# Kernel optimization log

Measured on AMD Instinct MI355X. Metric: run time of the kernel, lower is better.

The kernel has to match this reference:

```python
import jax, jax.numpy as jnp
import numpy as np

E, H, F = 1024, 16, 4096
WH, WW = 32, 32
B = 4
L = WH * WW           # 1024 cross-attn kv tokens
N = L + 1             # 1025 decoder tokens (CLS + window)
D = E // H
SCALE = D ** -0.5
NEG = -1e9            # stands in for -inf in the causal mask


def _rel_coords(Wh, Ww):
    coords = np.stack(np.meshgrid(np.arange(Wh), np.arange(Ww), indexing='ij')).reshape(2, -1)
    rc = (coords[:, :, None] - coords[:, None, :]).transpose(1, 2, 0).astype(np.int64)
    rc[:, :, 0] += Wh - 1
    rc[:, :, 1] += Ww - 1
    rc[:, :, 0] *= 2 * Ww - 1
    return rc.sum(-1)  # (L, L)


def rel_index_self(Wh, Ww):
    nrd = (2 * Wh - 1) * (2 * Ww - 1) + 3
    l = Wh * Ww
    idx = np.zeros((l + 1, l + 1), dtype=np.int32)
    idx[1:, 1:] = _rel_coords(Wh, Ww)
    idx[0, :] = nrd - 3
    idx[:, 0] = nrd - 2
    idx[0, 0] = nrd - 1
    return idx


def rel_index_cross(Wh, Ww):
    nrd = (2 * Wh - 1) * (2 * Ww - 1) + 1
    l = Wh * Ww
    idx = np.zeros((l + 1, l), dtype=np.int32)
    idx[1:, :] = _rel_coords(Wh, Ww)
    idx[0, :] = nrd - 1
    return idx


IDX_SELF = jnp.asarray(rel_index_self(WH, WW))    # (N, N) int32
IDX_CROSS = jnp.asarray(rel_index_cross(WH, WW))  # (N, L) int32
CAUSAL = jnp.triu(jnp.full((N, N), NEG, jnp.float32), 1)


def _ln(x, g, b, eps=1e-5):
    m = x.mean(-1, keepdims=True)
    v = ((x - m) ** 2).mean(-1, keepdims=True)
    return (x - m) * jax.lax.rsqrt(v + eps) * g + b


def setup_inputs():
    key = jax.random.key(0)
    ks = jax.random.split(key, 24)
    g = lambda i, shape, s=0.02: jax.random.normal(ks[i], shape, jnp.float32) * s
    return dict(
        x=g(0, (B, N, E), 1.0),
        y=g(1, (B, L, E), 1.0),
        norm1_g=jnp.ones((E,), jnp.float32), norm1_b=jnp.zeros((E,), jnp.float32),
        norm2_g=jnp.ones((E,), jnp.float32), norm2_b=jnp.zeros((E,), jnp.float32),
        norm3_g=jnp.ones((E,), jnp.float32), norm3_b=jnp.zeros((E,), jnp.float32),
        sa_qkv_w=g(2, (3 * E, E)),
        sa_q_bias=g(3, (E,)),
        sa_v_bias=g(4, (E,)),
        sa_rpb=g(5, ((2 * WH - 1) * (2 * WW - 1) + 3, H)),
        sa_proj_w=g(6, (E, E)), sa_proj_b=g(7, (E,)),
        ca_q_w=g(8, (E, E)),
        ca_kv_w=g(9, (2 * E, E)),
        ca_q_bias=g(10, (E,)),
        ca_v_bias=g(11, (E,)),
        ca_rpb=g(12, ((2 * WH - 1) * (2 * WW - 1) + 1, H)),
        ca_proj_w=g(13, (E, E)), ca_proj_b=g(14, (E,)),
        fc1_w=g(15, (F, E)), fc1_b=g(16, (F,)),
        fc2_w=g(17, (E, F)), fc2_b=g(18, (E,)),
        gamma1=jnp.full((E,), 0.1, jnp.float32),
        gamma2=jnp.full((E,), 0.1, jnp.float32),
        gamma3=jnp.full((E,), 0.1, jnp.float32),
    )


def reference(x, y, norm1_g, norm1_b, norm2_g, norm2_b, norm3_g, norm3_b,
              sa_qkv_w, sa_q_bias, sa_v_bias, sa_rpb, sa_proj_w, sa_proj_b,
              ca_q_w, ca_kv_w, ca_q_bias, ca_v_bias, ca_rpb, ca_proj_w, ca_proj_b,
              fc1_w, fc1_b, fc2_w, fc2_b, gamma1, gamma2, gamma3):
    # cross_attn.extract_kv(y): k gets zero bias, v gets v_bias
    kv_bias = jnp.concatenate([jnp.zeros((E,), x.dtype), ca_v_bias])
    kv = (y @ ca_kv_w.T + kv_bias).reshape(B, L, 2, H, D)
    ck = kv[:, :, 0].transpose(0, 2, 1, 3)  # (B,H,L,D)
    cv = kv[:, :, 1].transpose(0, 2, 1, 3)

    # --- causal self-attention with gathered relative-position bias ---
    h = _ln(x, norm1_g, norm1_b)
    qkv_bias = jnp.concatenate([sa_q_bias, jnp.zeros((E,), x.dtype), sa_v_bias])
    qkv = (h @ sa_qkv_w.T + qkv_bias).reshape(B, N, 3, H, D)
    q = qkv[:, :, 0].transpose(0, 2, 1, 3) * SCALE  # (B,H,N,D)
    k = qkv[:, :, 1].transpose(0, 2, 1, 3)
    v = qkv[:, :, 2].transpose(0, 2, 1, 3)
    bias = sa_rpb[IDX_SELF].transpose(2, 0, 1) + CAUSAL  # (H,N,N)
    attn = jnp.einsum('bhqd,bhkd->bhqk', q, k) + bias[None]
    attn = jax.nn.softmax(attn, axis=-1)
    sa = jnp.einsum('bhqk,bhkd->bhqd', attn, v).transpose(0, 2, 1, 3).reshape(B, N, E)
    sa = sa @ sa_proj_w.T + sa_proj_b
    x = x + gamma1 * sa

    # --- cross-attention with gathered relative-position bias ---
    h = _ln(x, norm2_g, norm2_b)
    q = (h @ ca_q_w.T + ca_q_bias).reshape(B, N, H, D).transpose(0, 2, 1, 3) * SCALE
    cbias = ca_rpb[IDX_CROSS].transpose(2, 0, 1)  # (H,N,L)
    attn = jnp.einsum('bhqd,bhkd->bhqk', q, ck) + cbias[None]
    attn = jax.nn.softmax(attn, axis=-1)
    ca = jnp.einsum('bhqk,bhkd->bhqd', attn, cv).transpose(0, 2, 1, 3).reshape(B, N, E)
    ca = ca @ ca_proj_w.T + ca_proj_b
    x = x + gamma2 * ca

    # --- FFN (Linear -> GELU -> Linear, no inner identity) ---
    h = _ln(x, norm3_g, norm3_b)
    h = jax.nn.gelu(h @ fc1_w.T + fc1_b, approximate=False)
    h = h @ fc2_w.T + fc2_b
    x = x + gamma3 * h
    return x
```

## Files before the change

kernel.cpp:

```cpp
#include <hip/hip_runtime.h>
#include <hip/hip_bf16.h>
#include <math.h>

typedef __bf16 bf16;
typedef __bf16 bf16x8 __attribute__((ext_vector_type(8)));
typedef float f32x4 __attribute__((ext_vector_type(4)));

#define MP    4224
#define MACT  4100
#define NQTOK 1025
#define NKTOK 1024
#define EDIM  1024
#define FDIM  4096
#define NHEAD 16
#define HD    64
#define QSCALE 0.125f
#define VTS   1056

__device__ __forceinline__ void glds16(const bf16* g, bf16* l) {
  __builtin_amdgcn_global_load_lds(
      (const __attribute__((address_space(1))) void*)g,
      (__attribute__((address_space(3))) void*)l, 16, 0, 0);
}

__device__ __forceinline__ bf16x8 ld8(const void* p, size_t i, bool f32) {
  if (f32) {
    const float* q = (const float*)p + i;
    bf16x8 r;
#pragma unroll
    for (int j = 0; j < 8; ++j) r[j] = (bf16)q[j];
    return r;
  }
  return *(const bf16x8*)((const bf16*)p + i);
}

struct WPtrs { const float* s[8]; };
__global__ __launch_bounds__(256) void conv_kernel(WPtrs wp, bf16* dst) {
  const size_t sz[8] = {3145728UL, 1048576UL, 1048576UL, 2097152UL,
                        1048576UL, 4194304UL, 4194304UL, 4194304UL};
  size_t id = ((size_t)blockIdx.x * 256 + threadIdx.x) * 8;
  size_t off = 0;
#pragma unroll
  for (int i = 0; i < 8; ++i) {
    if (id < off + sz[i]) {
      const float* s = wp.s[i] + (id - off);
      bf16x8 r;
#pragma unroll
      for (int j = 0; j < 8; ++j) r[j] = (bf16)s[j];
      *(bf16x8*)(dst + id) = r;
      return;
    }
    off += sz[i];
  }
}

__global__ void zero_pads_kernel(bf16* hln) {
  int i = blockIdx.x * 256 + threadIdx.x;
  const int n = (MP - MACT) * EDIM;
  if (i < n) hln[(size_t)MACT * EDIM + i] = (bf16)0.0f;
}

template<bool FIRST>
__global__ __launch_bounds__(256) void ln_kernel(const float* __restrict__ src,
    float* __restrict__ xf, bf16* __restrict__ out,
    const float* __restrict__ g, const float* __restrict__ bta) {
  const int row = blockIdx.x;
  const int tid = threadIdx.x;
  float v[4];
#pragma unroll
  for (int i = 0; i < 4; ++i) {
    v[i] = src[(size_t)row * EDIM + tid + i * 256];
    if (FIRST) xf[(size_t)row * EDIM + tid + i * 256] = v[i];
  }
  float s = 0.f, sq = 0.f;
#pragma unroll
  for (int i = 0; i < 4; ++i) { s += v[i]; sq += v[i] * v[i]; }
#pragma unroll
  for (int m = 32; m >= 1; m >>= 1) {
    s += __shfl_xor(s, m);
    sq += __shfl_xor(sq, m);
  }
  __shared__ float ss[4], ssq[4];
  const int wave = tid >> 6;
  if ((tid & 63) == 0) { ss[wave] = s; ssq[wave] = sq; }
  __syncthreads();
  s = ss[0] + ss[1] + ss[2] + ss[3];
  sq = ssq[0] + ssq[1] + ssq[2] + ssq[3];
  const float mean = s * (1.f / EDIM);
  const float var = sq * (1.f / EDIM) - mean * mean;
  const float rstd = rsqrtf(var + 1e-5f);
#pragma unroll
  for (int i = 0; i < 4; ++i) {
    int e = tid + i * 256;
    out[(size_t)row * EDIM + e] = (bf16)((v[i] - mean) * rstd * g[e] + bta[e]);
  }
}

__global__ __launch_bounds__(256) void fc2_reduce_kernel(
    const float* __restrict__ p0, const float* __restrict__ xf,
    const float* __restrict__ bias, const float* __restrict__ gamma,
    float* __restrict__ outf) {
  size_t i = ((size_t)blockIdx.x * 256 + threadIdx.x) * 4;
  if (i >= (size_t)MACT * EDIM) return;
  f32x4 a = *(const f32x4*)(p0 + i);
  f32x4 b = *(const f32x4*)(outf + i);
  f32x4 x = *(const f32x4*)(xf + i);
  const int gn = (int)(i & (EDIM - 1));
  f32x4 r;
#pragma unroll
  for (int j = 0; j < 4; ++j)
    r[j] = x[j] + gamma[gn + j] * (a[j] + b[j] + bias[gn + j]);
  *(f32x4*)(outf + i) = r;
}

enum { EPI_QKV = 0, EPI_KV = 1, EPI_Q = 2, EPI_RES = 3, EPI_GELU = 4,
       EPI_FINAL = 5, EPI_PART = 6 };

template<int EPI, bool ASY>
__global__ __launch_bounds__(256) void gemm_bt(
    const void* __restrict__ A, const void* __restrict__ Bw,
    int K, int Kc,
    const float* __restrict__ bias0, const float* __restrict__ bias1,
    const float* __restrict__ gamma, float* __restrict__ xf,
    bf16* __restrict__ out0, bf16* __restrict__ out1, bf16* __restrict__ out2,
    float* __restrict__ outf)
{
  constexpr int LDP = ASY ? 32 : 40;
  __shared__ bf16 As[2][128][LDP];
  __shared__ bf16 Bs[2][128][LDP];
  const int tid = threadIdx.x;
  const int lane = tid & 63, wave = tid >> 6;
  const int quad = lane >> 4, l16 = lane & 15;
  const int wr = wave >> 1, wc = wave & 1;
  const int m0 = blockIdx.y * 128, n0 = blockIdx.x * 128;
  const int kbase = blockIdx.z * Kc;
  const bool first = (blockIdx.z == 0);
  const int r0 = tid >> 2, c0 = (tid & 3) * 8;

  const bf16* gA = nullptr; const bf16* gB = nullptr;
  if (ASY) {
    gA = (const bf16*)A + (size_t)(m0 + wave * 16 + (lane >> 2)) * K + kbase + (lane & 3) * 8;
    gB = (const bf16*)Bw + (size_t)(n0 + wave * 16 + (lane >> 2)) * K + kbase + (lane & 3) * 8;
  }

  auto stage = [&](int bi, int kk) {
    if (ASY) {
      const bf16* pA = gA + kk;
      const bf16* pB = gB + kk;
      bf16* la = &As[bi][wave * 16][0];
      bf16* lb = &Bs[bi][wave * 16][0];
      glds16(pA, la);
      glds16(pA + (size_t)64 * K, la + 64 * LDP);
      glds16(pB, lb);
      glds16(pB + (size_t)64 * K, lb + 64 * LDP);
    } else {
      const bool f32a = (EPI == EPI_KV);
      const size_t kkk = (size_t)(kbase + kk);
      *(bf16x8*)(&As[bi][r0][c0])      = ld8(A,  (size_t)(m0 + r0) * K + kkk + c0, f32a);
      *(bf16x8*)(&As[bi][r0 + 64][c0]) = ld8(A,  (size_t)(m0 + r0 + 64) * K + kkk + c0, f32a);
      *(bf16x8*)(&Bs[bi][r0][c0])      = ld8(Bw, (size_t)(n0 + r0) * K + kkk + c0, true);
      *(bf16x8*)(&Bs[bi][r0 + 64][c0]) = ld8(Bw, (size_t)(n0 + r0 + 64) * K + kkk + c0, true);
    }
  };

  f32x4 acc[4][4];
#pragma unroll
  for (int i = 0; i < 4; ++i)
#pragma unroll
    for (int j = 0; j < 4; ++j)
#pragma unroll
      for (int r = 0; r < 4; ++r) acc[i][j][r] = 0.f;

  stage(0, 0);
  __syncthreads();
  int buf = 0;
  for (int k0 = 0; k0 < Kc; k0 += 32) {
    if (k0 + 32 < Kc) stage(buf ^ 1, k0 + 32);
    bf16x8 af[4], bfv[4];
#pragma unroll
    for (int i = 0; i < 4; ++i) {
      af[i]  = *(const bf16x8*)(&As[buf][wr * 64 + i * 16 + l16][quad * 8]);
      bfv[i] = *(const bf16x8*)(&Bs[buf][wc * 64 + i * 16 + l16][quad * 8]);
    }
#pragma unroll
    for (int mb = 0; mb < 4; ++mb)
#pragma unroll
      for (int nb = 0; nb < 4; ++nb)
        acc[mb][nb] = __builtin_amdgcn_mfma_f32_16x16x32_bf16(af[mb], bfv[nb], acc[mb][nb], 0, 0, 0);
    __syncthreads();
    buf ^= 1;
  }

#pragma unroll
  for (int mb = 0; mb < 4; ++mb) {
#pragma unroll
    for (int r = 0; r < 4; ++r) {
      const int gm = m0 + wr * 64 + mb * 16 + quad * 4 + r;
#pragma unroll
      for (int nb = 0; nb < 4; ++nb) {
        const int gn = n0 + wc * 64 + nb * 16 + l16;
        float v = acc[mb][nb][r];
        if (EPI == EPI_QKV) {
          if (gm < MACT) {
            unsigned b = (unsigned)gm / 1025u;
            unsigned t = (unsigned)gm - b * 1025u;
            int sec = gn >> 10, e = gn & 1023;
            int h = e >> 6, d = e & 63;
            if (sec == 0)
              out0[((size_t)(b * NHEAD + h) * NQTOK + t) * HD + d] =
                  (bf16)((v + bias0[e]) * QSCALE);
            else if (sec == 1)
              out1[((size_t)(b * NHEAD + h) * NQTOK + t) * HD + d] = (bf16)v;
            else
              out2[((size_t)(b * NHEAD + h) * HD + d) * VTS + t] =
                  (bf16)(v + bias1[e]);
          }
        } else if (EPI == EPI_KV) {
          unsigned b = (unsigned)gm >> 10;
          unsigned t = (unsigned)gm & 1023u;
          int sec = gn >> 10, e = gn & 1023;
          int h = e >> 6, d = e & 63;
          if (sec == 0)
            out0[((size_t)(b * NHEAD + h) * NKTOK + t) * HD + d] = (bf16)v;
          else
            out1[((size_t)(b * NHEAD + h) * HD + d) * NKTOK + t] =
                (bf16)(v + bias1[e]);
        } else if (EPI == EPI_Q) {
          if (gm < MACT) {
            unsigned b = (unsigned)gm / 1025u;
            unsigned t = (unsigned)gm - b * 1025u;
            int h = gn >> 6, d = gn & 63;
            outf[((size_t)(b * NHEAD + h) * NQTOK + t) * HD + d] =
                (v + bias0[gn]) * QSCALE;
          }
        } else if (EPI == EPI_RES) {
          if (gm < MACT) {
            size_t o = (size_t)gm * EDIM + gn;
            xf[o] += gamma[gn] * (v + bias0[gn]);
          }
        } else if (EPI == EPI_GELU) {
          float z = v + bias0[gn];
          float ge = 0.5f * z * (1.0f + erff(z * 0.70710678118f));
          out0[(size_t)gm * FDIM + gn] = (bf16)ge;
        } else if (EPI == EPI_PART) {
          if (gm < MACT) {
            float* dst = first ? xf : outf;
            dst[(size_t)gm * EDIM + gn] = v;
          }
        } else {
          if (gm < MACT) {
            size_t o = (size_t)gm * EDIM + gn;
            float add = gamma[gn] * (v + (first ? bias0[gn] : 0.f));
            if (first) add += xf[o];
            atomicAdd(&outf[o], add);
          }
        }
      }
    }
  }
}

template<bool CROSS>
__global__ __launch_bounds__(256) void attn_kernel(
    const void* __restrict__ Q, const bf16* __restrict__ Kg,
    const bf16* __restrict__ Vg, const float* __restrict__ rpb,
    bf16* __restrict__ out)
{
  const int NK  = CROSS ? NKTOK : NQTOK;
  const int NRD = CROSS ? 3970 : 3972;
  const int VS  = CROSS ? NKTOK : VTS;
  const int qt  = CROSS ? blockIdx.x : (16 - blockIdx.x);
  const int h = blockIdx.y, b = blockIdx.z;
  const int tid = threadIdx.x;
  const int lane = tid & 63, wave = tid >> 6;
  const int quad = lane >> 4, l16 = lane & 15;

  __shared__ bf16 rpb_s[4096];
  __shared__ bf16 Ks[64][72];
  __shared__ bf16 Vt[64][72];

  for (int i = tid; i < 4096; i += 256)
    rpb_s[i] = (bf16)((i < NRD) ? rpb[(size_t)i * NHEAD + h] : 0.f);

  const int q0 = qt * 64;
  const int qrow = q0 + wave * 16 + l16;
  const size_t qhb = (size_t)(b * NHEAD + h) * NQTOK;
  bf16x8 qf0, qf1;
  if (qrow < NQTOK) {
    if (CROSS) {
      const float* Qf = (const float*)Q + (qhb + qrow) * HD;
#pragma unroll
      for (int j = 0; j < 8; ++j) {
        qf0[j] = (bf16)Qf[quad * 8 + j];
        qf1[j] = (bf16)Qf[32 + quad * 8 + j];
      }
    } else {
      const bf16* Qb = (const bf16*)Q;
      qf0 = *(const bf16x8*)(Qb + (qhb + qrow) * HD + quad * 8);
      qf1 = *(const bf16x8*)(Qb + (qhb + qrow) * HD + 32 + quad * 8);
    }
  } else {
#pragma unroll
    for (int j = 0; j < 8; ++j) { qf0[j] = (bf16)0.f; qf1[j] = (bf16)0.f; }
  }

  const int qg = qrow;
  const int qp = qg - 1;
  const int qcode = (qg > 0) ? ((qp >> 5) * 63 + (qp & 31) + 1984) : 0;

  int ib[4][4];
#pragma unroll
  for (int kb = 0; kb < 4; ++kb)
#pragma unroll
    for (int r = 0; r < 4; ++r) {
      const int o = kb * 16 + quad * 4 + r;
      const int om = CROSS ? o : (o - 1);
      const int ocode = (om >> 5) * 63 + (om & 31);
      ib[kb][r] = qcode - ocode;
    }
  const bool q0cls = (q0 == 0);

  float m_run = -1e30f, l_run = 0.f;
  f32x4 oacc[4];
#pragma unroll
  for (int d = 0; d < 4; ++d)
#pragma unroll
    for (int r = 0; r < 4; ++r) oacc[d][r] = 0.f;

  const size_t kvbK = (size_t)(b * NHEAD + h) * NK;
  const size_t vbase = (size_t)(b * NHEAD + h) * HD;
  const int nch = CROSS ? (NKTOK / 64) : (qt + 1);

  const int rr = tid >> 3;
  const int co = (tid & 7) * 8;

  const int srcA = (quad & 1) * 32 + l16;
  const int srcB = srcA + 16;

  bf16x8 krg[2], vrg[2];
  auto stage_load = [&](int c) {
    const int kc = c * 64;
#pragma unroll
    for (int vv = 0; vv < 2; ++vv) {
      const int row = rr + vv * 32;
      if (!CROSS && kc + row >= NK) {
#pragma unroll
        for (int j = 0; j < 8; ++j) krg[vv][j] = (bf16)0.f;
      } else {
        krg[vv] = *(const bf16x8*)(Kg + (kvbK + kc + row) * HD + co);
      }
      if (!CROSS && kc + co >= NK) {
#pragma unroll
        for (int j = 0; j < 8; ++j) vrg[vv][j] = (bf16)0.f;
      } else {
        vrg[vv] = *(const bf16x8*)(Vg + (vbase + row) * VS + kc + co);
      }
    }
  };

  stage_load(0);
  int c126 = 0;
  for (int c = 0; c < nch; ++c) {
    const int kc = c * 64;
    if (c) __syncthreads();
#pragma unroll
    for (int vv = 0; vv < 2; ++vv) {
      const int row = rr + vv * 32;
      *(bf16x8*)(&Ks[row][co]) = krg[vv];
      *(bf16x8*)(&Vt[row][co]) = vrg[vv];
    }
    __syncthreads();
    if (c + 1 < nch) stage_load(c + 1);

    f32x4 aacc[4];
    __builtin_amdgcn_s_setprio(1);
#pragma unroll
    for (int kb = 0; kb < 4; ++kb) {
      bf16x8 kf0 = *(const bf16x8*)(&Ks[kb * 16 + l16][quad * 8]);
      bf16x8 kf1 = *(const bf16x8*)(&Ks[kb * 16 + l16][32 + quad * 8]);
      f32x4 a;
#pragma unroll
      for (int r = 0; r < 4; ++r) a[r] = 0.f;
      a = __builtin_amdgcn_mfma_f32_16x16x32_bf16(kf0, qf0, a, 0, 0, 0);
      a = __builtin_amdgcn_mfma_f32_16x16x32_bf16(kf1, qf1, a, 0, 0, 0);
      aacc[kb] = a;
    }
    __builtin_amdgcn_s_setprio(0);

    float sv[4][4];
    const bool lastc = (!CROSS) && (c == nch - 1);
    const bool firstc = (c == 0);
    if (!lastc) {
#pragma unroll
      for (int kb = 0; kb < 4; ++kb)
#pragma unroll
        for (int r = 0; r < 4; ++r) {
          int idx = ib[kb][r] - c126;
          if (q0cls) { if (qg == 0) idx = 3969; }
          if (!CROSS && firstc && kb == 0 && r == 0) {
            if (quad == 0) idx = (qg == 0) ? 3971 : 3970;
          }
          idx &= 4095;
          sv[kb][r] = aacc[kb][r] + (float)rpb_s[idx];
        }
    } else {
#pragma unroll
      for (int kb = 0; kb < 4; ++kb)
#pragma unroll
        for (int r = 0; r < 4; ++r) {
          int idx = ib[kb][r] - c126;
          if (q0cls) { if (qg == 0) idx = 3969; }
          if (firstc && kb == 0 && r == 0) {
            if (quad == 0) idx = (qg == 0) ? 3971 : 3970;
          }
          idx &= 4095;
          const int kg = kc + kb * 16 + quad * 4 + r;
          const bool valid = (kg < NK) && (kg <= qg);
          sv[kb][r] = valid ? (aacc[kb][r] + (float)rpb_s[idx]) : -1e30f;
        }
    }
    c126 += 126;

    float mx = sv[0][0];
#pragma unroll
    for (int kb = 0; kb < 4; ++kb)
#pragma unroll
      for (int r = 0; r < 4; ++r) mx = fmaxf(mx, sv[kb][r]);
    mx = fmaxf(mx, __shfl_xor(mx, 16));
    mx = fmaxf(mx, __shfl_xor(mx, 32));

    if (!__all(mx - m_run <= 8.f)) {
      const float mnew = fmaxf(m_run, mx);
      const float alpha = __expf(m_run - mnew);
      m_run = mnew;
      l_run *= alpha;
      float alr[4];
#pragma unroll
      for (int r = 0; r < 4; ++r) alr[r] = __shfl(alpha, quad * 4 + r);
#pragma unroll
      for (int d = 0; d < 4; ++d)
#pragma unroll
        for (int r = 0; r < 4; ++r) oacc[d][r] *= alr[r];
    }

    float rs = 0.f;
    unsigned pk[4][2];
#pragma unroll
    for (int kb = 0; kb < 4; ++kb) {
      float p0 = __expf(sv[kb][0] - m_run);
      float p1 = __expf(sv[kb][1] - m_run);
      float p2 = __expf(sv[kb][2] - m_run);
      float p3 = __expf(sv[kb][3] - m_run);
      rs += (p0 + p1) + (p2 + p3);
      union { __bf16 h[2]; unsigned u; } w0, w1;
      w0.h[0] = (bf16)p0; w0.h[1] = (bf16)p1;
      w1.h[0] = (bf16)p2; w1.h[1] = (bf16)p3;
      pk[kb][0] = w0.u; pk[kb][1] = w1.u;
    }
    rs += __shfl_xor(rs, 16);
    rs += __shfl_xor(rs, 32);
    l_run += rs;

    union { unsigned u[4]; bf16x8 v; } f0, f1;
#pragma unroll
    for (int p = 0; p < 4; ++p) {
      const int src = (p < 2) ? srcA : srcB;
      unsigned a0 = (unsigned)__shfl((int)pk[0][p & 1], src);
      unsigned a1 = (unsigned)__shfl((int)pk[1][p & 1], src);
      unsigned b0 = (unsigned)__shfl((int)pk[2][p & 1], src);
      unsigned b1 = (unsigned)__shfl((int)pk[3][p & 1], src);
      f0.u[p] = (quad < 2) ? a0 : a1;
      f1.u[p] = (quad < 2) ? b0 : b1;
    }

    __builtin_amdgcn_s_setprio(1);
#pragma unroll
    for (int db = 0; db < 4; ++db) {
      bf16x8 vf0 = *(const bf16x8*)(&Vt[db * 16 + l16][quad * 8]);
      bf16x8 vf1 = *(const bf16x8*)(&Vt[db * 16 + l16][32 + quad * 8]);
      oacc[db] = __builtin_amdgcn_mfma_f32_16x16x32_bf16(f0.v, vf0, oacc[db], 0, 0, 0);
      oacc[db] = __builtin_amdgcn_mfma_f32_16x16x32_bf16(f1.v, vf1, oacc[db], 0, 0, 0);
    }
    __builtin_amdgcn_s_setprio(0);
  }

#pragma unroll
  for (int r = 0; r < 4; ++r) {
    const int qo = q0 + wave * 16 + quad * 4 + r;
    if (qo < NQTOK) {
      const float inv = 1.f / __shfl(l_run, quad * 4 + r);
      const size_t row = (size_t)b * NQTOK + qo;
#pragma unroll
      for (int db = 0; db < 4; ++db)
        out[row * EDIM + h * HD + db * 16 + l16] = (bf16)(oacc[db][r] * inv);
    }
  }
}

extern "C" void kernel_launch(void* const* d_in, const int* in_sizes, int n_in,
                              void* d_out, int out_size, void* d_ws, size_t ws_size,
                              hipStream_t stream) {
  (void)in_sizes; (void)n_in; (void)out_size;
  const float* x        = (const float*)d_in[0];
  const float* y        = (const float*)d_in[1];
  const float* n1g      = (const float*)d_in[2];
  const float* n1b      = (const float*)d_in[3];
  const float* n2g      = (const float*)d_in[4];
  const float* n2b      = (const float*)d_in[5];
  const float* n3g      = (const float*)d_in[6];
  const float* n3b      = (const float*)d_in[7];
  const float* sa_qkv_w = (const float*)d_in[8];
  const float* sa_qb    = (const float*)d_in[9];
  const float* sa_vb    = (const float*)d_in[10];
  const float* sa_rpb   = (const float*)d_in[11];
  const float* sa_pw    = (const float*)d_in[12];
  const float* sa_pb    = (const float*)d_in[13];
  const float* ca_qw    = (const float*)d_in[14];
  const float* ca_kvw   = (const float*)d_in[15];
  const float* ca_qb    = (const float*)d_in[16];
  const float* ca_vb    = (const float*)d_in[17];
  const float* ca_rpb   = (const float*)d_in[18];
  const float* ca_pw    = (const float*)d_in[19];
  const float* ca_pb    = (const float*)d_in[20];
  const float* fc1_w    = (const float*)d_in[21];
  const float* fc1_b    = (const float*)d_in[22];
  const float* fc2_w    = (const float*)d_in[23];
  const float* fc2_b    = (const float*)d_in[24];
  const float* g1       = (const float*)d_in[25];
  const float* g2       = (const float*)d_in[26];
  const float* g3       = (const float*)d_in[27];
  float* outf = (float*)d_out;
  float* qtf  = (float*)d_out;

  char* w = (char*)d_ws;
  float* xf = (float*)w;  w += (size_t)MP * EDIM * 4;
  bf16* hln = (bf16*)w;   w += (size_t)MP * EDIM * 2;
  char* big = w;          w += (size_t)MP * FDIM * 2;
  const size_t qkv_sz = (size_t)4 * NHEAD * NQTOK * HD * 2;
  bf16* qt = (bf16*)big;
  bf16* kt = (bf16*)(big + qkv_sz);
  bf16* vt = (bf16*)(big + 2 * qkv_sz);
  bf16* h1 = (bf16*)big;
  bf16* wpool = (bf16*)w; w += 20971520UL * 2;
  const bool asy = ((size_t)(w - (char*)d_ws) <= ws_size);

  bf16* qkvw_b = wpool;
  bf16* pw_b   = qkvw_b + 3145728UL;
  bf16* cqw_b  = pw_b   + 1048576UL;
  bf16* ckvw_b = cqw_b  + 1048576UL;
  bf16* cpw_b  = ckvw_b + 2097152UL;
  bf16* fc1w_b = cpw_b  + 1048576UL;
  bf16* fc2w_b = fc1w_b + 4194304UL;
  bf16* y_b    = fc2w_b + 4194304UL;
  float* part0 = (float*)wpool;

  if (asy) {
    WPtrs wp = {{sa_qkv_w, sa_pw, ca_qw, ca_kvw, ca_pw, fc1_w, fc2_w, y}};
    conv_kernel<<<10240, 256, 0, stream>>>(wp, wpool);
  }
  zero_pads_kernel<<<dim3(((MP - MACT) * EDIM + 255) / 256), 256, 0, stream>>>(hln);

  ln_kernel<true><<<MACT, 256, 0, stream>>>(x, xf, hln, n1g, n1b);
  if (asy) gemm_bt<EPI_QKV, true><<<dim3(24, 33, 1), 256, 0, stream>>>(hln, qkvw_b, 1024, 1024,
      sa_qb, sa_vb, nullptr, nullptr, qt, kt, vt, nullptr);
  else     gemm_bt<EPI_QKV, false><<<dim3(24, 33, 1), 256, 0, stream>>>(hln, sa_qkv_w, 1024, 1024,
      sa_qb, sa_vb, nullptr, nullptr, qt, kt, vt, nullptr);
  attn_kernel<false><<<dim3(17, NHEAD, 4), 256, 0, stream>>>(qt, kt, vt, sa_rpb, hln);
  if (asy) gemm_bt<EPI_RES, true><<<dim3(8, 33, 1), 256, 0, stream>>>(hln, pw_b, 1024, 1024,
      sa_pb, nullptr, g1, xf, nullptr, nullptr, nullptr, nullptr);
  else     gemm_bt<EPI_RES, false><<<dim3(8, 33, 1), 256, 0, stream>>>(hln, sa_pw, 1024, 1024,
      sa_pb, nullptr, g1, xf, nullptr, nullptr, nullptr, nullptr);

  ln_kernel<false><<<MACT, 256, 0, stream>>>(xf, nullptr, hln, n2g, n2b);
  if (asy) gemm_bt<EPI_Q, true><<<dim3(8, 33, 1), 256, 0, stream>>>(hln, cqw_b, 1024, 1024,
      ca_qb, nullptr, nullptr, nullptr, nullptr, nullptr, nullptr, qtf);
  else     gemm_bt<EPI_Q, false><<<dim3(8, 33, 1), 256, 0, stream>>>(hln, ca_qw, 1024, 1024,
      ca_qb, nullptr, nullptr, nullptr, nullptr, nullptr, nullptr, qtf);
  if (asy) gemm_bt<EPI_KV, true><<<dim3(16, 32, 1), 256, 0, stream>>>(y_b, ckvw_b, 1024, 1024,
      nullptr, ca_vb, nullptr, nullptr, kt, vt, nullptr, nullptr);
  else     gemm_bt<EPI_KV, false><<<dim3(16, 32, 1), 256, 0, stream>>>(y, ca_kvw, 1024, 1024,
      nullptr, ca_vb, nullptr, nullptr, kt, vt, nullptr, nullptr);
  attn_kernel<true><<<dim3(17, NHEAD, 4), 256, 0, stream>>>(qtf, kt, vt, ca_rpb, hln);
  if (asy) gemm_bt<EPI_RES, true><<<dim3(8, 33, 1), 256, 0, stream>>>(hln, cpw_b, 1024, 1024,
      ca_pb, nullptr, g2, xf, nullptr, nullptr, nullptr, nullptr);
  else     gemm_bt<EPI_RES, false><<<dim3(8, 33, 1), 256, 0, stream>>>(hln, ca_pw, 1024, 1024,
      ca_pb, nullptr, g2, xf, nullptr, nullptr, nullptr, nullptr);

  ln_kernel<false><<<MACT, 256, 0, stream>>>(xf, nullptr, hln, n3g, n3b);
  if (asy) gemm_bt<EPI_GELU, true><<<dim3(32, 33, 1), 256, 0, stream>>>(hln, fc1w_b, 1024, 1024,
      fc1_b, nullptr, nullptr, nullptr, h1, nullptr, nullptr, nullptr);
  else     gemm_bt<EPI_GELU, false><<<dim3(32, 33, 1), 256, 0, stream>>>(hln, fc1_w, 1024, 1024,
      fc1_b, nullptr, nullptr, nullptr, h1, nullptr, nullptr, nullptr);
  if (asy) {
    gemm_bt<EPI_PART, true><<<dim3(8, 33, 2), 256, 0, stream>>>(h1, fc2w_b, 4096, 2048,
        nullptr, nullptr, nullptr, part0, nullptr, nullptr, nullptr, outf);
    fc2_reduce_kernel<<<dim3(4100), 256, 0, stream>>>(part0, xf, fc2_b, g3, outf);
  } else {
    hipMemsetAsync(outf, 0, (size_t)MACT * EDIM * 4, stream);
    gemm_bt<EPI_FINAL, false><<<dim3(8, 33, 4), 256, 0, stream>>>(h1, fc2_w, 4096, 1024,
        fc2_b, nullptr, g3, xf, nullptr, nullptr, nullptr, outf);
  }
}
```

Baseline: 678.5 us.

## Split attention KV loop across two blocks with log-sum-exp combine kernel

Both attention kernels now split each query tile's key/value chunks between two blocks (interleaved chunks), doubling the grid from 1088 to 2176 blocks. Each block writes a normalized partial output plus its running max and sum, and a new combine kernel merges the two halves into the final head-interleaved layout. The cross-attention Q projection now writes bf16 directly instead of fp32, which removes the per-element conversion in the attention kernel. The aim is better occupancy and less tail imbalance on the causal self-attention. The cost is an extra launch and extra partial-output traffic, and each block's software prefetch now covers only every other chunk.

```diff
diff --git a/kernel.cpp b/kernel.cpp
--- a/kernel.cpp
+++ b/kernel.cpp
@@ -16,6 +16,7 @@
 #define HD    64
 #define QSCALE 0.125f
 #define VTS   1056
+#define NROWS 65600
 
 __device__ __forceinline__ void glds16(const bf16* g, bf16* l) {
   __builtin_amdgcn_global_load_lds(
@@ -111,6 +112,35 @@
   for (int j = 0; j < 4; ++j)
     r[j] = x[j] + gamma[gn + j] * (a[j] + b[j] + bias[gn + j]);
   *(f32x4*)(outf + i) = r;
+}
+
+__global__ __launch_bounds__(256) void attn_combine_kernel(
+    const bf16* __restrict__ opart, const float* __restrict__ mlbuf,
+    bf16* __restrict__ out) {
+  const int tid = threadIdx.x;
+  const int row = blockIdx.x * 32 + (tid >> 3);
+  const int d0 = (tid & 7) * 8;
+  if (row >= NROWS) return;
+  const float m0 = mlbuf[(size_t)row * 2],           l0 = mlbuf[(size_t)row * 2 + 1];
+  const float m1 = mlbuf[((size_t)NROWS + row) * 2], l1 = mlbuf[((size_t)NROWS + row) * 2 + 1];
+  const float M = fmaxf(m0, m1);
+  float w0 = __expf(m0 - M) * l0;
+  float w1 = __expf(m1 - M) * l1;
+  const float den = w0 + w1;
+  const float sc = (den > 0.f) ? 1.f / den : 0.f;
+  w0 *= sc; w1 *= sc;
+  const size_t OPSZ = (size_t)NROWS * HD;
+  bf16x8 a = *(const bf16x8*)(opart + (size_t)row * HD + d0);
+  bf16x8 c = *(const bf16x8*)(opart + OPSZ + (size_t)row * HD + d0);
+  const int b = row / (NHEAD * NQTOK);
+  const int rem = row - b * (NHEAD * NQTOK);
+  const int h = rem / NQTOK;
+  const int q = rem - h * NQTOK;
+  bf16x8 o;
+#pragma unroll
+  for (int j = 0; j < 8; ++j)
+    o[j] = (bf16)(w0 * (float)a[j] + w1 * (float)c[j]);
+  *(bf16x8*)(out + ((size_t)b * NQTOK + q) * EDIM + h * HD + d0) = o;
 }
 
 enum { EPI_QKV = 0, EPI_KV = 1, EPI_Q = 2, EPI_RES = 3, EPI_GELU = 4,
@@ -230,8 +260,8 @@
             unsigned b = (unsigned)gm / 1025u;
             unsigned t = (unsigned)gm - b * 1025u;
             int h = gn >> 6, d = gn & 63;
-            outf[((size_t)(b * NHEAD + h) * NQTOK + t) * HD + d] =
-                (v + bias0[gn]) * QSCALE;
+            out0[((size_t)(b * NHEAD + h) * NQTOK + t) * HD + d] =
+                (bf16)((v + bias0[gn]) * QSCALE);
           }
         } else if (EPI == EPI_RES) {
           if (gm < MACT) {
@@ -262,15 +292,16 @@
 
 template<bool CROSS>
 __global__ __launch_bounds__(256) void attn_kernel(
-    const void* __restrict__ Q, const bf16* __restrict__ Kg,
+    const bf16* __restrict__ Qg, const bf16* __restrict__ Kg,
     const bf16* __restrict__ Vg, const float* __restrict__ rpb,
-    bf16* __restrict__ out)
+    bf16* __restrict__ opart, float* __restrict__ mlbuf)
 {
   const int NK  = CROSS ? NKTOK : NQTOK;
   const int NRD = CROSS ? 3970 : 3972;
   const int VS  = CROSS ? NKTOK : VTS;
   const int qt  = CROSS ? blockIdx.x : (16 - blockIdx.x);
-  const int h = blockIdx.y, b = blockIdx.z;
+  const int h = blockIdx.y;
+  const int b = blockIdx.z & 3, s = blockIdx.z >> 2;
   const int tid = threadIdx.x;
   const int lane = tid & 63, wave = tid >> 6;
   const int quad = lane >> 4, l16 = lane & 15;
@@ -287,18 +318,8 @@
   const size_t qhb = (size_t)(b * NHEAD + h) * NQTOK;
   bf16x8 qf0, qf1;
   if (qrow < NQTOK) {
-    if (CROSS) {
-      const float* Qf = (const float*)Q + (qhb + qrow) * HD;
-#pragma unroll
-      for (int j = 0; j < 8; ++j) {
-        qf0[j] = (bf16)Qf[quad * 8 + j];
-        qf1[j] = (bf16)Qf[32 + quad * 8 + j];
-      }
-    } else {
-      const bf16* Qb = (const bf16*)Q;
-      qf0 = *(const bf16x8*)(Qb + (qhb + qrow) * HD + quad * 8);
-      qf1 = *(const bf16x8*)(Qb + (qhb + qrow) * HD + 32 + quad * 8);
-    }
+    qf0 = *(const bf16x8*)(Qg + (qhb + qrow) * HD + quad * 8);
+    qf1 = *(const bf16x8*)(Qg + (qhb + qrow) * HD + 32 + quad * 8);
   } else {
 #pragma unroll
     for (int j = 0; j < 8; ++j) { qf0[j] = (bf16)0.f; qf1[j] = (bf16)0.f; }
@@ -358,11 +379,11 @@
     }
   };
 
-  stage_load(0);
-  int c126 = 0;
-  for (int c = 0; c < nch; ++c) {
+  if (s < nch) stage_load(s);
+  int c126 = s * 126;
+  for (int c = s; c < nch; c += 2) {
     const int kc = c * 64;
-    if (c) __syncthreads();
+    if (c != s) __syncthreads();
 #pragma unroll
     for (int vv = 0; vv < 2; ++vv) {
       const int row = rr + vv * 32;
@@ -370,7 +391,7 @@
       *(bf16x8*)(&Vt[row][co]) = vrg[vv];
     }
     __syncthreads();
-    if (c + 1 < nch) stage_load(c + 1);
+    if (c + 2 < nch) stage_load(c + 2);
 
     f32x4 aacc[4];
     __builtin_amdgcn_s_setprio(1);
@@ -419,7 +440,7 @@
           sv[kb][r] = valid ? (aacc[kb][r] + (float)rpb_s[idx]) : -1e30f;
         }
     }
-    c126 += 126;
+    c126 += 252;
 
     float mx = sv[0][0];
 #pragma unroll
@@ -484,16 +505,24 @@
     __builtin_amdgcn_s_setprio(0);
   }
 
+  const size_t OPSZ = (size_t)NROWS * HD;
 #pragma unroll
   for (int r = 0; r < 4; ++r) {
     const int qo = q0 + wave * 16 + quad * 4 + r;
     if (qo < NQTOK) {
-      const float inv = 1.f / __shfl(l_run, quad * 4 + r);
-      const size_t row = (size_t)b * NQTOK + qo;
+      const float lr = __shfl(l_run, quad * 4 + r);
+      const float inv = (lr > 0.f) ? 1.f / lr : 0.f;
+      const size_t orow = (size_t)(b * NHEAD + h) * NQTOK + qo;
 #pragma unroll
       for (int db = 0; db < 4; ++db)
-        out[row * EDIM + h * HD + db * 16 + l16] = (bf16)(oacc[db][r] * inv);
-    }
+        opart[(size_t)s * OPSZ + orow * HD + db * 16 + l16] =
+            (bf16)(oacc[db][r] * inv);
+    }
+  }
+  if (quad == 0 && qrow < NQTOK) {
+    const size_t orow = (size_t)(b * NHEAD + h) * NQTOK + qrow;
+    mlbuf[((size_t)s * NROWS + orow) * 2 + 0] = m_run;
+    mlbuf[((size_t)s * NROWS + orow) * 2 + 1] = l_run;
   }
 }
 
@@ -530,7 +559,7 @@
   const float* g2       = (const float*)d_in[26];
   const float* g3       = (const float*)d_in[27];
   float* outf = (float*)d_out;
-  float* qtf  = (float*)d_out;
+  bf16* opart = (bf16*)d_out;
 
   char* w = (char*)d_ws;
   float* xf = (float*)w;  w += (size_t)MP * EDIM * 4;
@@ -541,6 +570,7 @@
   bf16* kt = (bf16*)(big + qkv_sz);
   bf16* vt = (bf16*)(big + 2 * qkv_sz);
   bf16* h1 = (bf16*)big;
+  float* mlf = (float*)(big + 26214400UL);
   bf16* wpool = (bf16*)w; w += 20971520UL * 2;
   const bool asy = ((size_t)(w - (char*)d_ws) <= ws_size);
 
@@ -565,7 +595,8 @@
       sa_qb, sa_vb, nullptr, nullptr, qt, kt, vt, nullptr);
   else     gemm_bt<EPI_QKV, false><<<dim3(24, 33, 1), 256, 0, stream>>>(hln, sa_qkv_w, 1024, 1024,
       sa_qb, sa_vb, nullptr, nullptr, qt, kt, vt, nullptr);
-  attn_kernel<false><<<dim3(17, NHEAD, 4), 256, 0, stream>>>(qt, kt, vt, sa_rpb, hln);
+  attn_kernel<false><<<dim3(17, NHEAD, 8), 256, 0, stream>>>(qt, kt, vt, sa_rpb, opart, mlf);
+  attn_combine_kernel<<<dim3(NROWS / 32), 256, 0, stream>>>(opart, mlf, hln);
   if (asy) gemm_bt<EPI_RES, true><<<dim3(8, 33, 1), 256, 0, stream>>>(hln, pw_b, 1024, 1024,
       sa_pb, nullptr, g1, xf, nullptr, nullptr, nullptr, nullptr);
   else     gemm_bt<EPI_RES, false><<<dim3(8, 33, 1), 256, 0, stream>>>(hln, sa_pw, 1024, 1024,
@@ -573,14 +604,15 @@
 
   ln_kernel<false><<<MACT, 256, 0, stream>>>(xf, nullptr, hln, n2g, n2b);
   if (asy) gemm_bt<EPI_Q, true><<<dim3(8, 33, 1), 256, 0, stream>>>(hln, cqw_b, 1024, 1024,
-      ca_qb, nullptr, nullptr, nullptr, nullptr, nullptr, nullptr, qtf);
+      ca_qb, nullptr, nullptr, nullptr, qt, nullptr, nullptr, nullptr);
   else     gemm_bt<EPI_Q, false><<<dim3(8, 33, 1), 256, 0, stream>>>(hln, ca_qw, 1024, 1024,
-      ca_qb, nullptr, nullptr, nullptr, nullptr, nullptr, nullptr, qtf);
+      ca_qb, nullptr, nullptr, nullptr, qt, nullptr, nullptr, nullptr);
   if (asy) gemm_bt<EPI_KV, true><<<dim3(16, 32, 1), 256, 0, stream>>>(y_b, ckvw_b, 1024, 1024,
       nullptr, ca_vb, nullptr, nullptr, kt, vt, nullptr, nullptr);
   else     gemm_bt<EPI_KV, false><<<dim3(16, 32, 1), 256, 0, stream>>>(y, ca_kvw, 1024, 1024,
       nullptr, ca_vb, nullptr, nullptr, kt, vt, nullptr, nullptr);
-  attn_kernel<true><<<dim3(17, NHEAD, 4), 256, 0, stream>>>(qtf, kt, vt, ca_rpb, hln);
+  attn_kernel<true><<<dim3(17, NHEAD, 8), 256, 0, stream>>>(qt, kt, vt, ca_rpb, opart, mlf);
+  attn_combine_kernel<<<dim3(NROWS / 32), 256, 0, stream>>>(opart, mlf, hln);
   if (asy) gemm_bt<EPI_RES, true><<<dim3(8, 33, 1), 256, 0, stream>>>(hln, cpw_b, 1024, 1024,
       ca_pb, nullptr, g2, xf, nullptr, nullptr, nullptr, nullptr);
   else     gemm_bt<EPI_RES, false><<<dim3(8, 33, 1), 256, 0, stream>>>(hln, ca_pw, 1024, 1024,
```

New measurement: 675.2 us. Within noise of the previous version (-0.5%).
